# Kernel tuning notes

Measured on AMD Instinct MI355X. Metric: run time of the kernel, lower is better.

The kernel has to match this reference:

```python
import jax, jax.numpy as jnp
import numpy as np

N_DRUG = 20000
N_PROT = 30000
N = N_DRUG + N_PROT
F_DRUG = 128
F_PROT = 256
H = 64          # hidden_channels
OUT = 1         # out_channels
E = 1_600_000
L = 200_000
LAYERS = 3


def _lin_init(key, fan_in, fan_out):
    return jax.random.normal(key, (fan_in, fan_out), jnp.float32) / np.sqrt(fan_in)


def setup_inputs() -> dict:
    key = jax.random.key(0)
    ks = jax.random.split(key, 10)
    x_drug = jax.random.normal(ks[0], (N_DRUG, F_DRUG), jnp.float32)
    x_protein = jax.random.normal(ks[1], (N_PROT, F_PROT), jnp.float32)
    edge_index = jax.random.randint(ks[2], (2, E), 0, N, dtype=jnp.int64)
    edge_label_src = jax.random.randint(ks[3], (L,), 0, N_DRUG, dtype=jnp.int64)
    # protein label indices point into the concatenated [drug; protein] tensor
    edge_label_dst = jax.random.randint(ks[4], (L,), 0, N_PROT, dtype=jnp.int64) + N_DRUG
    W_drug = _lin_init(ks[5], F_DRUG, H)
    b_drug = jnp.zeros((H,), jnp.float32)
    W_prot = _lin_init(ks[6], F_PROT, H)
    b_prot = jnp.zeros((H,), jnp.float32)
    conv_W = jax.random.normal(ks[7], (LAYERS, H, H), jnp.float32) / np.sqrt(H)
    conv_b = jnp.zeros((LAYERS, H), jnp.float32)
    lin_W = _lin_init(ks[8], H, OUT)
    lin_b = jnp.zeros((OUT,), jnp.float32)
    return {
        "x_drug": x_drug, "x_protein": x_protein,
        "W_drug": W_drug, "b_drug": b_drug,
        "W_prot": W_prot, "b_prot": b_prot,
        "conv_W": conv_W, "conv_b": conv_b,
        "lin_W": lin_W, "lin_b": lin_b,
        "edge_index": edge_index,
        "edge_label_src": edge_label_src,
        "edge_label_dst": edge_label_dst,
    }


def reference(x_drug, x_protein, W_drug, b_drug, W_prot, b_prot,
              conv_W, conv_b, lin_W, lin_b,
              edge_index, edge_label_src, edge_label_dst):
    # type-specific input projections + relu
    hd = jax.nn.relu(x_drug @ W_drug + b_drug)
    hp = jax.nn.relu(x_protein @ W_prot + b_prot)
    x = jnp.concatenate([hd, hp], axis=0)  # [N, H]

    src, dst = edge_index[0], edge_index[1]
    # GCN normalization with self-loops: deg counts in-edges (by dst) + 1
    deg = jax.ops.segment_sum(jnp.ones_like(src, dtype=x.dtype), dst, num_segments=N) + 1.0
    dis = jax.lax.rsqrt(deg)               # deg >= 1 always
    edge_norm = (dis[src] * dis[dst])[:, None]   # [E, 1]
    self_norm = (dis * dis)[:, None]             # [N, 1]

    for l in range(LAYERS):
        xw = x @ conv_W[l]                                   # [N, H] dense GEMM
        agg = jax.ops.segment_sum(xw[src] * edge_norm, dst, num_segments=N)
        x = jax.nn.relu(agg + xw * self_norm + conv_b[l])

    # edge scoring head: gather endpoints, linear to 1, multiply, sigmoid
    sd = (x[edge_label_src] @ lin_W + lin_b)[:, 0]  # [L]
    sp = (x[edge_label_dst] @ lin_W + lin_b)[:, 0]  # [L]
    return jax.nn.sigmoid(sd * sp)
```

## Files before the change

### kernel.cpp

```cpp
#include <hip/hip_runtime.h>
#include <hip/hip_fp16.h>
#include <math.h>

#define N_DRUG 20000
#define N_PROT 30000
#define NN (N_DRUG + N_PROT)
#define F_DRUG 128
#define F_PROT 256
#define H 64
#define NE 1600000
#define NL 200000

#define NB_PROJD ((N_DRUG + 255) / 256)
#define NB_PROJP ((N_PROT + 255) / 256)
#define NB_CONV  ((NN + 255) / 256)
#define NB_ROW4  (NN / 4)
#define NBK1 256
#define CH   ((NE + NBK1 - 1) / NBK1)
#define NB_BKT ((NN + 255) / 256)

typedef _Float16 h8 __attribute__((ext_vector_type(8)));
typedef _Float16 h4 __attribute__((ext_vector_type(4)));
typedef float f32x4 __attribute__((ext_vector_type(4)));

#define MFMA16(a, b, c) __builtin_amdgcn_mfma_f32_16x16x32_f16((a), (b), (c), 0, 0, 0)

__global__ __launch_bounds__(256) void k_wprep(
    const float* __restrict__ Wd, const float* __restrict__ Wp,
    const float* __restrict__ cw,
    _Float16* __restrict__ wdt, _Float16* __restrict__ wpt,
    _Float16* __restrict__ cwt) {
    int i = blockIdx.x * 256 + threadIdx.x;
    if (i < 64 * F_DRUG) {
        int c = i / F_DRUG, k = i % F_DRUG;
        wdt[i] = (_Float16)Wd[k * H + c];
    }
    if (i < 64 * F_PROT) {
        int c = i / F_PROT, k = i % F_PROT;
        wpt[i] = (_Float16)Wp[k * H + c];
    }
    if (i < 3 * 64 * 64) {
        int l = i >> 12, r = i & 4095;
        int c = r >> 6, k = r & 63;
        cwt[i] = (_Float16)cw[(l << 12) + k * H + c];
    }
}

template <int F>
__device__ __forceinline__ void proj_direct(
    const float* __restrict__ X, const _Float16* __restrict__ Wt,
    const float* __restrict__ bias, _Float16* __restrict__ out,
    int rows, int row_off, int bid) {
    int l = threadIdx.x & 63, wvi = threadIdx.x >> 6;
    int lr = l & 15, lq = l >> 4;
    int r0 = bid * 256 + wvi * 64;
    f32x4 acc[4][4];
    #pragma unroll
    for (int rt = 0; rt < 4; ++rt)
        #pragma unroll
        for (int n = 0; n < 4; ++n) acc[rt][n] = (f32x4){0.f, 0.f, 0.f, 0.f};

    for (int k0 = 0; k0 < F; k0 += 64) {
        h8 af[4][2];
        #pragma unroll
        for (int n = 0; n < 4; ++n)
            #pragma unroll
            for (int kk = 0; kk < 2; ++kk)
                af[n][kk] = *(const h8*)&Wt[(size_t)(n * 16 + lr) * F + k0 + kk * 32 + lq * 8];
        #pragma unroll
        for (int rt = 0; rt < 4; ++rt) {
            int r = r0 + rt * 16 + lr;
            int rc = (r < rows) ? r : (rows - 1);
            h8 bf[2];
            #pragma unroll
            for (int kk = 0; kk < 2; ++kk) {
                const float* xp = X + (size_t)rc * F + k0 + kk * 32 + lq * 8;
                float4 a = *(const float4*)xp;
                float4 b = *(const float4*)(xp + 4);
                h8 t;
                t[0] = (_Float16)a.x; t[1] = (_Float16)a.y;
                t[2] = (_Float16)a.z; t[3] = (_Float16)a.w;
                t[4] = (_Float16)b.x; t[5] = (_Float16)b.y;
                t[6] = (_Float16)b.z; t[7] = (_Float16)b.w;
                bf[kk] = t;
            }
            #pragma unroll
            for (int n = 0; n < 4; ++n) {
                acc[rt][n] = MFMA16(af[n][0], bf[0], acc[rt][n]);
                acc[rt][n] = MFMA16(af[n][1], bf[1], acc[rt][n]);
            }
        }
    }
    #pragma unroll
    for (int rt = 0; rt < 4; ++rt) {
        int r = r0 + rt * 16 + lr;
        if (r < rows) {
            #pragma unroll
            for (int n = 0; n < 4; ++n) {
                int c = n * 16 + lq * 4;
                float4 bv = *(const float4*)&bias[c];
                h4 hv;
                hv[0] = (_Float16)fmaxf(acc[rt][n][0] + bv.x, 0.f);
                hv[1] = (_Float16)fmaxf(acc[rt][n][1] + bv.y, 0.f);
                hv[2] = (_Float16)fmaxf(acc[rt][n][2] + bv.z, 0.f);
                hv[3] = (_Float16)fmaxf(acc[rt][n][3] + bv.w, 0.f);
                *(h4*)(out + (size_t)(row_off + r) * H + c) = hv;
            }
        }
    }
}

__device__ __forceinline__ void conv_direct(
    const _Float16* __restrict__ xh, const _Float16* __restrict__ Wt,
    _Float16* __restrict__ xout, int bid) {
    int l = threadIdx.x & 63, wvi = threadIdx.x >> 6;
    int lr = l & 15, lq = l >> 4;
    h8 af[4][2];
    #pragma unroll
    for (int n = 0; n < 4; ++n)
        #pragma unroll
        for (int kk = 0; kk < 2; ++kk)
            af[n][kk] = *(const h8*)&Wt[(size_t)(n * 16 + lr) * 64 + kk * 32 + lq * 8];
    int r0 = bid * 256 + wvi * 64;
    #pragma unroll
    for (int rt = 0; rt < 4; ++rt) {
        int r = r0 + rt * 16 + lr;
        int rc = (r < NN) ? r : (NN - 1);
        h8 bf0 = *(const h8*)&xh[(size_t)rc * H + lq * 8];
        h8 bf1 = *(const h8*)&xh[(size_t)rc * H + 32 + lq * 8];
        f32x4 a[4];
        #pragma unroll
        for (int n = 0; n < 4; ++n) {
            a[n] = (f32x4){0.f, 0.f, 0.f, 0.f};
            a[n] = MFMA16(af[n][0], bf0, a[n]);
            a[n] = MFMA16(af[n][1], bf1, a[n]);
        }
        if (r < NN) {
            #pragma unroll
            for (int n = 0; n < 4; ++n) {
                int c = n * 16 + lq * 4;
                h4 hv;
                hv[0] = (_Float16)a[n][0]; hv[1] = (_Float16)a[n][1];
                hv[2] = (_Float16)a[n][2]; hv[3] = (_Float16)a[n][3];
                *(h4*)(xout + (size_t)r * H + c) = hv;
            }
        }
    }
}

__global__ __launch_bounds__(256) void k_front(
    const float* __restrict__ xd, const _Float16* __restrict__ wdt, const float* __restrict__ bd,
    const float* __restrict__ xp, const _Float16* __restrict__ wpt, const float* __restrict__ bp,
    const int* __restrict__ ei, unsigned* __restrict__ bhist, _Float16* __restrict__ xa) {
    __shared__ unsigned lh[256];
    int bid = blockIdx.x;
    if (bid < NB_PROJD) {
        proj_direct<F_DRUG>(xd, wdt, bd, xa, N_DRUG, 0, bid);
    } else if (bid < NB_PROJD + NB_PROJP) {
        proj_direct<F_PROT>(xp, wpt, bp, xa, N_PROT, N_DRUG, bid - NB_PROJD);
    } else {
        int blk = bid - NB_PROJD - NB_PROJP;
        int t = threadIdx.x;
        lh[t] = 0;
        __syncthreads();
        int eb = blk * CH, ee = min(NE, eb + CH);
        for (int e = eb + t; e < ee; e += 256)
            atomicAdd(&lh[((unsigned)ei[NE + e]) >> 8], 1u);
        __syncthreads();
        bhist[(size_t)t * NBK1 + blk] = lh[t];
    }
}

__global__ __launch_bounds__(256) void kA(const unsigned* __restrict__ bhist,
                                          unsigned* __restrict__ rsum) {
    __shared__ unsigned s[256];
    int j = blockIdx.x, t = threadIdx.x;
    s[t] = bhist[(size_t)j * NBK1 + t];
    __syncthreads();
    for (int off = 128; off; off >>= 1) {
        if (t < off) s[t] += s[t + off];
        __syncthreads();
    }
    if (t == 0) rsum[j] = s[0];
}

__global__ __launch_bounds__(256) void kC2(unsigned* __restrict__ bhist,
                                           const unsigned* __restrict__ rsum,
                                           unsigned* __restrict__ rbase) {
    __shared__ unsigned sb[256], s[256];
    int j = blockIdx.x, t = threadIdx.x;
    unsigned rc = rsum[t];
    sb[t] = rc;
    __syncthreads();
    for (int off = 1; off < 256; off <<= 1) {
        unsigned v = sb[t]; unsigned u = (t >= off) ? sb[t - off] : 0;
        __syncthreads(); sb[t] = v + u; __syncthreads();
    }
    if (j == 0) {
        rbase[t] = sb[t] - rc;
        if (t == 255) rbase[256] = sb[255];
    }
    unsigned rb = (j > 0) ? sb[j - 1] : 0;
    unsigned c = bhist[(size_t)j * NBK1 + t];
    s[t] = c;
    __syncthreads();
    for (int off = 1; off < 256; off <<= 1) {
        unsigned v = s[t]; unsigned u = (t >= off) ? s[t - off] : 0;
        __syncthreads(); s[t] = v + u; __syncthreads();
    }
    bhist[(size_t)j * NBK1 + t] = rb + s[t] - c;
}

__global__ __launch_bounds__(256) void k_part(
    const int* __restrict__ ei, const unsigned* __restrict__ base,
    unsigned* __restrict__ tmp) {
    __shared__ unsigned lcur[256];
    int bid = blockIdx.x;
    int c = ((bid & 7) << 5) | (bid >> 3);
    int t = threadIdx.x;
    lcur[t] = base[(size_t)t * NBK1 + c];
    __syncthreads();
    int eb = c * CH, ee = min(NE, eb + CH);
    for (int e = eb + t; e < ee; e += 256) {
        unsigned s = (unsigned)ei[e];
        unsigned d = (unsigned)ei[NE + e];
        unsigned pos = atomicAdd(&lcur[d >> 8], 1u);
        tmp[pos] = ((d & 255u) << 16) | s;
    }
}

__global__ __launch_bounds__(256) void k_csrconv(
    const unsigned* __restrict__ tmp, const unsigned* __restrict__ rbase,
    int* __restrict__ rp, float* __restrict__ dis, unsigned short* __restrict__ csr,
    const _Float16* __restrict__ xa, const _Float16* __restrict__ cwt,
    _Float16* __restrict__ xw) {
    __shared__ unsigned lbin[256], lofs[256], lcur[256];
    int bid = blockIdx.x;
    if (bid >= NB_BKT) {
        conv_direct(xa, cwt, xw, bid - NB_BKT);
        return;
    }
    int b = bid, t = threadIdx.x;
    unsigned nb0 = rbase[b], nb1 = rbase[b + 1];
    lbin[t] = 0;
    __syncthreads();
    for (unsigned i = nb0 + t; i < nb1; i += 256)
        atomicAdd(&lbin[tmp[i] >> 16], 1u);
    __syncthreads();
    unsigned c = lbin[t];
    lofs[t] = c;
    __syncthreads();
    for (int off = 1; off < 256; off <<= 1) {
        unsigned v = lofs[t]; unsigned u = (t >= off) ? lofs[t - off] : 0;
        __syncthreads(); lofs[t] = v + u; __syncthreads();
    }
    unsigned r = nb0 + lofs[t] - c;
    int node = b * 256 + t;
    if (node < NN) {
        rp[node] = (int)r;
        dis[node] = rsqrtf((float)c + 1.0f);
    }
    lcur[t] = r;
    __syncthreads();
    for (unsigned i = nb0 + t; i < nb1; i += 256) {
        unsigned rec = tmp[i];
        unsigned pos = atomicAdd(&lcur[rec >> 16], 1u);
        csr[pos] = (unsigned short)(rec & 0xffffu);
    }
    if (b == 0 && t == 0) rp[NN] = NE;
}

__global__ __launch_bounds__(256) void k_conv(
    const _Float16* __restrict__ X, const _Float16* __restrict__ Wt,
    _Float16* __restrict__ out) {
    conv_direct(X, Wt, out, blockIdx.x);
}

template <bool FIRST, bool LAST>
__global__ __launch_bounds__(256) void k_spmm4(
    const int* __restrict__ rp, const unsigned short* __restrict__ csr,
    unsigned* __restrict__ pack, const float* __restrict__ dis,
    const _Float16* __restrict__ xin,
    const float* __restrict__ bias, _Float16* __restrict__ xout,
    const float* __restrict__ lw, const float* __restrict__ lb,
    float* __restrict__ y) {
    int lane = threadIdx.x & 63;
    int d = blockIdx.x * 4 + (threadIdx.x >> 6);
    int o = lane >> 3, g = lane & 7;
    int beg = rp[d], end = rp[d + 1];
    float dd = dis[d];
    float acc[8];
    #pragma unroll
    for (int i = 0; i < 8; ++i) acc[i] = 0.f;

    int n = end - beg; if (n > 64) n = 64;
    unsigned rv = 0;
    if (lane < n) {
        if (FIRST) {
            int s = csr[beg + lane];
            float w0 = dis[s] * dd;
            rv = (unsigned)s | ((unsigned)__half_as_ushort(__float2half(w0)) << 16);
            pack[beg + lane] = rv;
        } else rv = pack[beg + lane];
    }
    for (int b0 = beg; b0 < end; ) {
        int nb = b0 + 64;
        int n2 = end - nb; if (n2 > 64) n2 = 64;
        unsigned rv2 = 0;
        if (n2 > 0 && lane < n2) {
            if (FIRST) {
                int s = csr[nb + lane];
                float w0 = dis[s] * dd;
                rv2 = (unsigned)s | ((unsigned)__half_as_ushort(__float2half(w0)) << 16);
                pack[nb + lane] = rv2;
            } else rv2 = pack[nb + lane];
        }
        int nsteps = (n + 7) >> 3;
        #pragma unroll 4
        for (int jj = 0; jj < nsteps; ++jj) {
            unsigned r = __shfl(rv, jj * 8 + o);
            float w = __half2float(__ushort_as_half((unsigned short)(r >> 16)));
            h8 xv = *(const h8*)&xin[((r & 0xffffu) << 6) + (g << 3)];
            #pragma unroll
            for (int i = 0; i < 8; ++i) acc[i] += w * (float)xv[i];
        }
        b0 = nb; n = n2; rv = rv2;
    }
    #pragma unroll
    for (int off = 8; off < 64; off <<= 1)
        #pragma unroll
        for (int i = 0; i < 8; ++i) acc[i] += __shfl_xor(acc[i], off);
    h8 xs = *(const h8*)&xin[((unsigned)d << 6) + (g << 3)];
    float sn = dd * dd;
    #pragma unroll
    for (int i = 0; i < 8; ++i) acc[i] += sn * (float)xs[i];

    if (LAST) {
        float4 l0 = *(const float4*)&lw[g << 3];
        float4 l1 = *(const float4*)&lw[(g << 3) + 4];
        float t = acc[0] * l0.x + acc[1] * l0.y + acc[2] * l0.z + acc[3] * l0.w
                + acc[4] * l1.x + acc[5] * l1.y + acc[6] * l1.z + acc[7] * l1.w;
        t += __shfl_xor(t, 1); t += __shfl_xor(t, 2); t += __shfl_xor(t, 4);
        if (lane == 0) y[d] = t + lb[0];
    } else if (o == 0) {
        float4 b0 = *(const float4*)&bias[g << 3];
        float4 b1 = *(const float4*)&bias[(g << 3) + 4];
        h8 hv;
        hv[0] = (_Float16)fmaxf(acc[0] + b0.x, 0.f);
        hv[1] = (_Float16)fmaxf(acc[1] + b0.y, 0.f);
        hv[2] = (_Float16)fmaxf(acc[2] + b0.z, 0.f);
        hv[3] = (_Float16)fmaxf(acc[3] + b0.w, 0.f);
        hv[4] = (_Float16)fmaxf(acc[4] + b1.x, 0.f);
        hv[5] = (_Float16)fmaxf(acc[5] + b1.y, 0.f);
        hv[6] = (_Float16)fmaxf(acc[6] + b1.z, 0.f);
        hv[7] = (_Float16)fmaxf(acc[7] + b1.w, 0.f);
        *(h8*)(xout + ((size_t)d << 6) + (g << 3)) = hv;
    }
}

__global__ void k_out(const float* __restrict__ y, const int* __restrict__ ls,
                      const int* __restrict__ ld, float* __restrict__ out) {
    int e = blockIdx.x * blockDim.x + threadIdx.x;
    if (e < NL) {
        float z = y[ls[e]] * y[ld[e]];
        out[e] = 1.f / (1.f + __expf(-z));
    }
}

static inline size_t up256(size_t x) { return (x + 255) & ~(size_t)255; }

extern "C" void kernel_launch(void* const* d_in, const int* in_sizes, int n_in,
                              void* d_out, int out_size, void* d_ws, size_t ws_size,
                              hipStream_t stream) {
    const float* x_drug = (const float*)d_in[0];
    const float* x_prot = (const float*)d_in[1];
    const float* W_drug = (const float*)d_in[2];
    const float* b_drug = (const float*)d_in[3];
    const float* W_prot = (const float*)d_in[4];
    const float* b_prot = (const float*)d_in[5];
    const float* conv_W = (const float*)d_in[6];
    const float* conv_b = (const float*)d_in[7];
    const float* lin_W  = (const float*)d_in[8];
    const float* lin_b  = (const float*)d_in[9];
    const int*   ei     = (const int*)d_in[10];
    const int*   lsrc   = (const int*)d_in[11];
    const int*   ldst   = (const int*)d_in[12];
    float* out = (float*)d_out;

    char* w = (char*)d_ws;
    size_t off = 0;
    unsigned* bhist = (unsigned*)(w + off); off = up256(off + (size_t)256 * NBK1 * 4);
    unsigned* rsum  = (unsigned*)(w + off); off = up256(off + 256 * 4);
    unsigned* rbase = (unsigned*)(w + off); off = up256(off + 257 * 4);
    unsigned* tmp   = (unsigned*)(w + off); off = up256(off + (size_t)NE * 4);
    unsigned short* csr = (unsigned short*)(w + off); off = up256(off + (size_t)NE * 2);
    unsigned* pack  = (unsigned*)(w + off); off = up256(off + (size_t)NE * 4);
    int*    rp   = (int*)(w + off);    off = up256(off + (size_t)(NN + 1) * 4);
    float*  dis  = (float*)(w + off);  off = up256(off + (size_t)NN * 4);
    _Float16* xa = (_Float16*)(w + off); off = up256(off + (size_t)NN * H * 2);
    _Float16* xb = (_Float16*)(w + off); off = up256(off + (size_t)NN * H * 2);
    _Float16* xw = (_Float16*)(w + off); off = up256(off + (size_t)NN * H * 2);
    float*  y    = (float*)(w + off);  off = up256(off + (size_t)NN * 4);
    _Float16* wdt = (_Float16*)(w + off); off = up256(off + (size_t)64 * F_DRUG * 2);
    _Float16* wpt = (_Float16*)(w + off); off = up256(off + (size_t)64 * F_PROT * 2);
    _Float16* cwt = (_Float16*)(w + off); off = up256(off + (size_t)3 * 64 * 64 * 2);

    k_wprep<<<64, 256, 0, stream>>>(W_drug, W_prot, conv_W, wdt, wpt, cwt);

    k_front<<<NB_PROJD + NB_PROJP + NBK1, 256, 0, stream>>>(
        x_drug, wdt, b_drug, x_prot, wpt, b_prot, ei, bhist, xa);

    kA<<<256, 256, 0, stream>>>(bhist, rsum);
    kC2<<<256, 256, 0, stream>>>(bhist, rsum, rbase);

    k_part<<<NBK1, 256, 0, stream>>>(ei, bhist, tmp);

    k_csrconv<<<NB_BKT + NB_CONV, 256, 0, stream>>>(
        tmp, rbase, rp, dis, csr, xa, cwt, xw);

    k_spmm4<true, false><<<NB_ROW4, 256, 0, stream>>>(
        rp, csr, pack, dis, xw, conv_b, xb, nullptr, nullptr, nullptr);
    k_conv<<<NB_CONV, 256, 0, stream>>>(xb, cwt + 4096, xw);
    k_spmm4<false, false><<<NB_ROW4, 256, 0, stream>>>(
        rp, csr, pack, dis, xw, conv_b + 64, xa, nullptr, nullptr, nullptr);
    k_conv<<<NB_CONV, 256, 0, stream>>>(xa, cwt + 8192, xw);
    k_spmm4<false, true><<<NB_ROW4, 256, 0, stream>>>(
        rp, csr, pack, dis, xw, conv_b + 128, nullptr, lin_W, lin_b, y);

    k_out<<<(NL + 255) / 256, 256, 0, stream>>>(y, lsrc, ldst, out);
}
```

Before: 182.0 us.

## Fuse next-layer dense GEMM into SpMM epilogue with MFMA on 16-row tiles

Each SpMM block now aggregates 16 destination rows (4 per wave) and stages the relu'd result in swizzled shared memory. An MFMA 16x16x32 tile then multiplies it by the next layer's weight and writes XW directly. This removes the separate conv kernels, and with them the global write and re-read of the intermediate activations plus two launches. Each wave now processes rows serially, giving fewer and larger blocks, and a block barrier is added. The last layer now also applies bias and relu before the output linear, which corrects the earlier epilogue.

```diff
diff --git a/kernel.cpp b/kernel.cpp
--- a/kernel.cpp
+++ b/kernel.cpp
@@ -14,7 +14,7 @@
 #define NB_PROJD ((N_DRUG + 255) / 256)
 #define NB_PROJP ((N_PROT + 255) / 256)
 #define NB_CONV  ((NN + 255) / 256)
-#define NB_ROW4  (NN / 4)
+#define NB_ROW16 (NN / 16)
 #define NBK1 256
 #define CH   ((NE + NBK1 - 1) / NBK1)
 #define NB_BKT ((NN + 255) / 256)
@@ -270,91 +270,116 @@
     if (b == 0 && t == 0) rp[NN] = NE;
 }
 
-__global__ __launch_bounds__(256) void k_conv(
-    const _Float16* __restrict__ X, const _Float16* __restrict__ Wt,
-    _Float16* __restrict__ out) {
-    conv_direct(X, Wt, out, blockIdx.x);
-}
-
 template <bool FIRST, bool LAST>
-__global__ __launch_bounds__(256) void k_spmm4(
+__global__ __launch_bounds__(256) void k_spmm5(
     const int* __restrict__ rp, const unsigned short* __restrict__ csr,
     unsigned* __restrict__ pack, const float* __restrict__ dis,
-    const _Float16* __restrict__ xin,
-    const float* __restrict__ bias, _Float16* __restrict__ xout,
+    const _Float16* __restrict__ xin, const _Float16* __restrict__ Wt,
+    const float* __restrict__ bias, _Float16* __restrict__ xwout,
     const float* __restrict__ lw, const float* __restrict__ lb,
     float* __restrict__ y) {
-    int lane = threadIdx.x & 63;
-    int d = blockIdx.x * 4 + (threadIdx.x >> 6);
+    __shared__ _Float16 v[16 * 64];
+    int lane = threadIdx.x & 63, wvi = threadIdx.x >> 6;
     int o = lane >> 3, g = lane & 7;
-    int beg = rp[d], end = rp[d + 1];
-    float dd = dis[d];
-    float acc[8];
+    int d0 = blockIdx.x * 16;
+
     #pragma unroll
-    for (int i = 0; i < 8; ++i) acc[i] = 0.f;
-
-    int n = end - beg; if (n > 64) n = 64;
-    unsigned rv = 0;
-    if (lane < n) {
-        if (FIRST) {
-            int s = csr[beg + lane];
-            float w0 = dis[s] * dd;
-            rv = (unsigned)s | ((unsigned)__half_as_ushort(__float2half(w0)) << 16);
-            pack[beg + lane] = rv;
-        } else rv = pack[beg + lane];
-    }
-    for (int b0 = beg; b0 < end; ) {
-        int nb = b0 + 64;
-        int n2 = end - nb; if (n2 > 64) n2 = 64;
-        unsigned rv2 = 0;
-        if (n2 > 0 && lane < n2) {
+    for (int rr = 0; rr < 4; ++rr) {
+        int d = d0 + wvi * 4 + rr;
+        int beg = rp[d], end = rp[d + 1];
+        float dd = dis[d];
+        float acc[8];
+        #pragma unroll
+        for (int i = 0; i < 8; ++i) acc[i] = 0.f;
+
+        int n = end - beg; if (n > 64) n = 64;
+        unsigned rv = 0;
+        if (lane < n) {
             if (FIRST) {
-                int s = csr[nb + lane];
+                int s = csr[beg + lane];
                 float w0 = dis[s] * dd;
-                rv2 = (unsigned)s | ((unsigned)__half_as_ushort(__float2half(w0)) << 16);
-                pack[nb + lane] = rv2;
-            } else rv2 = pack[nb + lane];
-        }
-        int nsteps = (n + 7) >> 3;
-        #pragma unroll 4
-        for (int jj = 0; jj < nsteps; ++jj) {
-            unsigned r = __shfl(rv, jj * 8 + o);
-            float w = __half2float(__ushort_as_half((unsigned short)(r >> 16)));
-            h8 xv = *(const h8*)&xin[((r & 0xffffu) << 6) + (g << 3)];
-            #pragma unroll
-            for (int i = 0; i < 8; ++i) acc[i] += w * (float)xv[i];
-        }
-        b0 = nb; n = n2; rv = rv2;
-    }
-    #pragma unroll
-    for (int off = 8; off < 64; off <<= 1)
-        #pragma unroll
-        for (int i = 0; i < 8; ++i) acc[i] += __shfl_xor(acc[i], off);
-    h8 xs = *(const h8*)&xin[((unsigned)d << 6) + (g << 3)];
-    float sn = dd * dd;
-    #pragma unroll
-    for (int i = 0; i < 8; ++i) acc[i] += sn * (float)xs[i];
-
-    if (LAST) {
-        float4 l0 = *(const float4*)&lw[g << 3];
-        float4 l1 = *(const float4*)&lw[(g << 3) + 4];
-        float t = acc[0] * l0.x + acc[1] * l0.y + acc[2] * l0.z + acc[3] * l0.w
-                + acc[4] * l1.x + acc[5] * l1.y + acc[6] * l1.z + acc[7] * l1.w;
-        t += __shfl_xor(t, 1); t += __shfl_xor(t, 2); t += __shfl_xor(t, 4);
-        if (lane == 0) y[d] = t + lb[0];
-    } else if (o == 0) {
-        float4 b0 = *(const float4*)&bias[g << 3];
-        float4 b1 = *(const float4*)&bias[(g << 3) + 4];
-        h8 hv;
-        hv[0] = (_Float16)fmaxf(acc[0] + b0.x, 0.f);
-        hv[1] = (_Float16)fmaxf(acc[1] + b0.y, 0.f);
-        hv[2] = (_Float16)fmaxf(acc[2] + b0.z, 0.f);
-        hv[3] = (_Float16)fmaxf(acc[3] + b0.w, 0.f);
-        hv[4] = (_Float16)fmaxf(acc[4] + b1.x, 0.f);
-        hv[5] = (_Float16)fmaxf(acc[5] + b1.y, 0.f);
-        hv[6] = (_Float16)fmaxf(acc[6] + b1.z, 0.f);
-        hv[7] = (_Float16)fmaxf(acc[7] + b1.w, 0.f);
-        *(h8*)(xout + ((size_t)d << 6) + (g << 3)) = hv;
+                rv = (unsigned)s | ((unsigned)__half_as_ushort(__float2half(w0)) << 16);
+                pack[beg + lane] = rv;
+            } else rv = pack[beg + lane];
+        }
+        for (int b0 = beg; b0 < end; ) {
+            int nb = b0 + 64;
+            int n2 = end - nb; if (n2 > 64) n2 = 64;
+            unsigned rv2 = 0;
+            if (n2 > 0 && lane < n2) {
+                if (FIRST) {
+                    int s = csr[nb + lane];
+                    float w0 = dis[s] * dd;
+                    rv2 = (unsigned)s | ((unsigned)__half_as_ushort(__float2half(w0)) << 16);
+                    pack[nb + lane] = rv2;
+                } else rv2 = pack[nb + lane];
+            }
+            int nsteps = (n + 7) >> 3;
+            #pragma unroll 4
+            for (int jj = 0; jj < nsteps; ++jj) {
+                unsigned r = __shfl(rv, jj * 8 + o);
+                float w = __half2float(__ushort_as_half((unsigned short)(r >> 16)));
+                h8 xv = *(const h8*)&xin[((r & 0xffffu) << 6) + (g << 3)];
+                #pragma unroll
+                for (int i = 0; i < 8; ++i) acc[i] += w * (float)xv[i];
+            }
+            b0 = nb; n = n2; rv = rv2;
+        }
+        #pragma unroll
+        for (int off = 8; off < 64; off <<= 1)
+            #pragma unroll
+            for (int i = 0; i < 8; ++i) acc[i] += __shfl_xor(acc[i], off);
+        h8 xs = *(const h8*)&xin[((unsigned)d << 6) + (g << 3)];
+        float sn = dd * dd;
+        #pragma unroll
+        for (int i = 0; i < 8; ++i) acc[i] += sn * (float)xs[i];
+
+        if (LAST) {
+            float4 b0v = *(const float4*)&bias[g << 3];
+            float4 b1v = *(const float4*)&bias[(g << 3) + 4];
+            float vv[8];
+            vv[0] = fmaxf(acc[0] + b0v.x, 0.f); vv[1] = fmaxf(acc[1] + b0v.y, 0.f);
+            vv[2] = fmaxf(acc[2] + b0v.z, 0.f); vv[3] = fmaxf(acc[3] + b0v.w, 0.f);
+            vv[4] = fmaxf(acc[4] + b1v.x, 0.f); vv[5] = fmaxf(acc[5] + b1v.y, 0.f);
+            vv[6] = fmaxf(acc[6] + b1v.z, 0.f); vv[7] = fmaxf(acc[7] + b1v.w, 0.f);
+            float4 l0 = *(const float4*)&lw[g << 3];
+            float4 l1 = *(const float4*)&lw[(g << 3) + 4];
+            float t = vv[0] * l0.x + vv[1] * l0.y + vv[2] * l0.z + vv[3] * l0.w
+                    + vv[4] * l1.x + vv[5] * l1.y + vv[6] * l1.z + vv[7] * l1.w;
+            t += __shfl_xor(t, 1); t += __shfl_xor(t, 2); t += __shfl_xor(t, 4);
+            if (lane == 0) y[d] = t + lb[0];
+        } else if (o == 0) {
+            float4 b0v = *(const float4*)&bias[g << 3];
+            float4 b1v = *(const float4*)&bias[(g << 3) + 4];
+            h8 hv;
+            hv[0] = (_Float16)fmaxf(acc[0] + b0v.x, 0.f);
+            hv[1] = (_Float16)fmaxf(acc[1] + b0v.y, 0.f);
+            hv[2] = (_Float16)fmaxf(acc[2] + b0v.z, 0.f);
+            hv[3] = (_Float16)fmaxf(acc[3] + b0v.w, 0.f);
+            hv[4] = (_Float16)fmaxf(acc[4] + b1v.x, 0.f);
+            hv[5] = (_Float16)fmaxf(acc[5] + b1v.y, 0.f);
+            hv[6] = (_Float16)fmaxf(acc[6] + b1v.z, 0.f);
+            hv[7] = (_Float16)fmaxf(acc[7] + b1v.w, 0.f);
+            int rl = wvi * 4 + rr;
+            *(h8*)&v[rl * 64 + ((g ^ (rl & 7)) << 3)] = hv;
+        }
+    }
+
+    if (!LAST) {
+        __syncthreads();
+        int lr = lane & 15, lq = lane >> 4;
+        h8 af0 = *(const h8*)&Wt[(size_t)(wvi * 16 + lr) * 64 + lq * 8];
+        h8 af1 = *(const h8*)&Wt[(size_t)(wvi * 16 + lr) * 64 + 32 + lq * 8];
+        h8 bf0 = *(const h8*)&v[lr * 64 + ((lq ^ (lr & 7)) << 3)];
+        h8 bf1 = *(const h8*)&v[lr * 64 + (((4 + lq) ^ (lr & 7)) << 3)];
+        f32x4 a = (f32x4){0.f, 0.f, 0.f, 0.f};
+        a = MFMA16(af0, bf0, a);
+        a = MFMA16(af1, bf1, a);
+        int c = wvi * 16 + lq * 4;
+        h4 hv;
+        hv[0] = (_Float16)a[0]; hv[1] = (_Float16)a[1];
+        hv[2] = (_Float16)a[2]; hv[3] = (_Float16)a[3];
+        *(h4*)(xwout + (size_t)(d0 + lr) * H + c) = hv;
     }
 }
 
@@ -418,14 +443,12 @@
     k_csrconv<<<NB_BKT + NB_CONV, 256, 0, stream>>>(
         tmp, rbase, rp, dis, csr, xa, cwt, xw);
 
-    k_spmm4<true, false><<<NB_ROW4, 256, 0, stream>>>(
-        rp, csr, pack, dis, xw, conv_b, xb, nullptr, nullptr, nullptr);
-    k_conv<<<NB_CONV, 256, 0, stream>>>(xb, cwt + 4096, xw);
-    k_spmm4<false, false><<<NB_ROW4, 256, 0, stream>>>(
-        rp, csr, pack, dis, xw, conv_b + 64, xa, nullptr, nullptr, nullptr);
-    k_conv<<<NB_CONV, 256, 0, stream>>>(xa, cwt + 8192, xw);
-    k_spmm4<false, true><<<NB_ROW4, 256, 0, stream>>>(
-        rp, csr, pack, dis, xw, conv_b + 128, nullptr, lin_W, lin_b, y);
+    k_spmm5<true, false><<<NB_ROW16, 256, 0, stream>>>(
+        rp, csr, pack, dis, xw, cwt + 4096, conv_b, xb, nullptr, nullptr, nullptr);
+    k_spmm5<false, false><<<NB_ROW16, 256, 0, stream>>>(
+        rp, csr, pack, dis, xb, cwt + 8192, conv_b + 64, xa, nullptr, nullptr, nullptr);
+    k_spmm5<false, true><<<NB_ROW16, 256, 0, stream>>>(
+        rp, csr, pack, dis, xa, nullptr, conv_b + 128, nullptr, lin_W, lin_b, y);
 
     k_out<<<(NL + 255) / 256, 256, 0, stream>>>(y, lsrc, ldst, out);
 }
```

Result: faster. 174.1 us (-4.3%).
